# Kernel optimization log

Hardware: AMD Instinct MI355X
Metric: run time of the kernel (lower is better)

The kernel has to match this reference:

```python
import jax, jax.numpy as jnp
import numpy as np

N_NODES = 100000
N_EDGES = 1600000
IN_FEATS = 128
HIDDEN = 128
NUM_CLASSES = 2
EDGE_FEAT = 1


def setup_inputs() -> dict:
    key = jax.random.key(0)
    ks = jax.random.split(key, 24)
    s = 0.05
    inp = {
        "node_feats": jax.random.normal(ks[0], (N_NODES, IN_FEATS), jnp.float32),
        "edge_feats": jax.random.normal(ks[1], (N_EDGES, EDGE_FEAT), jnp.float32),
        "src": jax.random.randint(ks[2], (N_EDGES,), 0, N_NODES),
        "dst": jax.random.randint(ks[3], (N_EDGES,), 0, N_NODES),
        # SAGEConv layer 0: in -> hidden
        "ws0": jax.random.normal(ks[4], (IN_FEATS, HIDDEN), jnp.float32) * s,
        "wn0": jax.random.normal(ks[5], (IN_FEATS, HIDDEN), jnp.float32) * s,
        "b0": jnp.zeros((HIDDEN,), jnp.float32),
        # SAGEConv layer 1: hidden -> hidden
        "ws1": jax.random.normal(ks[6], (HIDDEN, HIDDEN), jnp.float32) * s,
        "wn1": jax.random.normal(ks[7], (HIDDEN, HIDDEN), jnp.float32) * s,
        "b1": jnp.zeros((HIDDEN,), jnp.float32),
        # SAGEConv layer 2: hidden -> hidden
        "ws2": jax.random.normal(ks[8], (HIDDEN, HIDDEN), jnp.float32) * s,
        "wn2": jax.random.normal(ks[9], (HIDDEN, HIDDEN), jnp.float32) * s,
        "b2": jnp.zeros((HIDDEN,), jnp.float32),
        # edge MLP
        "mw1": jax.random.normal(ks[10], (2 * HIDDEN + EDGE_FEAT, HIDDEN), jnp.float32) * s,
        "mb1": jnp.zeros((HIDDEN,), jnp.float32),
        "mw2": jax.random.normal(ks[11], (HIDDEN, NUM_CLASSES), jnp.float32) * s,
        "mb2": jnp.zeros((NUM_CLASSES,), jnp.float32),
    }
    return inp


def _sage_mean(h, src, dst, inv_deg, w_self, w_neigh, b, n_nodes):
    # mean over incoming edges of source features, per destination node
    agg = jax.ops.segment_sum(h[src], dst, num_segments=n_nodes)
    mean_neigh = agg * inv_deg
    return h @ w_self + mean_neigh @ w_neigh + b


def reference(node_feats, edge_feats, src, dst,
              ws0, wn0, b0, ws1, wn1, b1, ws2, wn2, b2,
              mw1, mb1, mw2, mb2):
    n_nodes = node_feats.shape[0]
    deg = jax.ops.segment_sum(jnp.ones_like(dst, dtype=node_feats.dtype), dst,
                              num_segments=n_nodes)
    inv_deg = (1.0 / jnp.maximum(deg, 1.0))[:, None]

    h = node_feats
    for (ws, wn, b) in ((ws0, wn0, b0), (ws1, wn1, b1), (ws2, wn2, b2)):
        h = _sage_mean(h, src, dst, inv_deg, ws, wn, b, n_nodes)
        h = jax.nn.leaky_relu(h, negative_slope=0.01)
        # dropout is identity in eval mode

    # edge gather + concat + MLP
    edge_repr = jnp.concatenate([h[src], h[dst], edge_feats], axis=1)
    hidden = jax.nn.relu(edge_repr @ mw1 + mb1)
    logits = hidden @ mw2 + mb2
    return logits
```

## Files before the change

kernel.cpp:

```cpp
#include <hip/hip_runtime.h>
#include <hip/hip_bf16.h>

#define N_NODES 100000
#define N_EDGES 1600000
#define F 128
#define KW 272
#define KS 144
#define KD 128
#define EROUNDS 8
#define NBUCK 512
#define BCAP 5120
#define NB 98
#define CHUNK 8192
#define NSBLK ((N_EDGES + CHUNK - 1) / CHUNK)

typedef short bf16x8 __attribute__((ext_vector_type(8)));
typedef float f32x16 __attribute__((ext_vector_type(16)));
typedef _Float16 half8 __attribute__((ext_vector_type(8)));
typedef _Float16 half4 __attribute__((ext_vector_type(4)));

__device__ __forceinline__ short f2bf(float x) {
    unsigned u = __builtin_bit_cast(unsigned, x);
    u += 0x7FFF + ((u >> 16) & 1);
    return (short)(u >> 16);
}
__device__ __forceinline__ float bflo(unsigned u) {
    return __builtin_bit_cast(float, u << 16);
}
__device__ __forceinline__ float bfhi(unsigned u) {
    return __builtin_bit_cast(float, u & 0xFFFF0000u);
}
__device__ __forceinline__ void acc8(float* a, uint4 u) {
    a[0] += bflo(u.x); a[1] += bfhi(u.x);
    a[2] += bflo(u.y); a[3] += bfhi(u.y);
    a[4] += bflo(u.z); a[5] += bfhi(u.z);
    a[6] += bflo(u.w); a[7] += bfhi(u.w);
}

__global__ __launch_bounds__(256) void bucket_scatter(
    const int* __restrict__ src, const int* __restrict__ dst,
    int* __restrict__ bcur, unsigned* __restrict__ bstore) {
    __shared__ int hist[NBUCK];
    __shared__ unsigned pk[CHUNK];
    int t = threadIdx.x;
    int e0 = blockIdx.x * CHUNK;
    int n = N_EDGES - e0; if (n > CHUNK) n = CHUNK;
    for (int i = t; i < NBUCK; i += 256) hist[i] = 0;
    __syncthreads();
    for (int i = t; i < n; i += 256) {
        int d = dst[e0 + i];
        int s = src[e0 + i];
        pk[i] = ((unsigned)(d & 255) << 17) | (unsigned)s;
        atomicAdd(&hist[d >> 8], 1);
    }
    __syncthreads();
    for (int i = t; i < NBUCK; i += 256) {
        int c = hist[i];
        hist[i] = (c > 0) ? atomicAdd(&bcur[i], c) : 0;
    }
    __syncthreads();
    for (int i = t; i < n; i += 256) {
        int bk = dst[e0 + i] >> 8;
        int p = atomicAdd(&hist[bk], 1);
        if (p < BCAP) bstore[(size_t)bk * BCAP + p] = pk[i];
    }
}

__global__ __launch_bounds__(256) void bucket_deg(const unsigned* __restrict__ bstore,
                                                  const int* __restrict__ bcur,
                                                  int* __restrict__ deg) {
    __shared__ int cnt[256];
    int b = blockIdx.x, t = threadIdx.x;
    cnt[t] = 0;
    __syncthreads();
    int n = bcur[b]; if (n > BCAP) n = BCAP;
    const unsigned* p = bstore + (size_t)b * BCAP;
    for (int i = t; i < n; i += 256) atomicAdd(&cnt[p[i] >> 17], 1);
    __syncthreads();
    int node = b * 256 + t;
    if (node < N_NODES) deg[node] = cnt[t];
}

__global__ __launch_bounds__(1024) void scan1_kernel(const int* __restrict__ deg,
                                                     int* __restrict__ incl,
                                                     int* __restrict__ bsum) {
    __shared__ int wsum[16];
    int t = threadIdx.x, lane = t & 63, wid = t >> 6;
    int i = blockIdx.x * 1024 + t;
    int v = (i < N_NODES) ? deg[i] : 0;
    int sc = v;
#pragma unroll
    for (int off = 1; off < 64; off <<= 1) {
        int u = __shfl_up(sc, off, 64);
        if (lane >= off) sc += u;
    }
    if (lane == 63) wsum[wid] = sc;
    __syncthreads();
    if (wid == 0) {
        int wv = (lane < 16) ? wsum[lane] : 0;
        int wi = wv;
#pragma unroll
        for (int off = 1; off < 16; off <<= 1) {
            int u = __shfl_up(wi, off, 64);
            if (lane >= off) wi += u;
        }
        if (lane < 16) wsum[lane] = wi - wv;
    }
    __syncthreads();
    int full = sc + wsum[wid];
    if (i < N_NODES) incl[i] = full;
    if (t == 1023) bsum[blockIdx.x] = full;
}

__global__ void scan2_kernel(const int* __restrict__ bsum, int* __restrict__ boff,
                             int* __restrict__ row_ptr) {
    __shared__ int w0;
    int t = threadIdx.x, lane = t & 63, wid = t >> 6;
    int v = (t < NB) ? bsum[t] : 0;
    int sc = v;
#pragma unroll
    for (int off = 1; off < 64; off <<= 1) {
        int u = __shfl_up(sc, off, 64);
        if (lane >= off) sc += u;
    }
    if (wid == 0 && lane == 63) w0 = sc;
    __syncthreads();
    if (wid == 1) sc += w0;
    if (t < NB) boff[t] = sc - v;
    if (t == NB - 1) row_ptr[N_NODES] = sc;
}

__global__ __launch_bounds__(1024) void scan3_kernel(const int* __restrict__ incl,
                                                     const int* __restrict__ deg,
                                                     const int* __restrict__ boff,
                                                     int* __restrict__ row_ptr,
                                                     float* __restrict__ invd) {
    int i = blockIdx.x * 1024 + threadIdx.x;
    if (i >= N_NODES) return;
    int d = deg[i];
    row_ptr[i] = incl[i] - d + boff[blockIdx.x];
    invd[i] = 1.0f / (float)(d > 1 ? d : 1);
}

__global__ __launch_bounds__(256) void bucket_fill(const unsigned* __restrict__ bstore,
                                                   const int* __restrict__ bcur,
                                                   const int* __restrict__ row_ptr,
                                                   int* __restrict__ csr_src) {
    __shared__ int cur[256];
    int b = blockIdx.x, t = threadIdx.x;
    int node = b * 256 + t;
    cur[t] = (node < N_NODES) ? row_ptr[node] : 0;
    __syncthreads();
    int n = bcur[b]; if (n > BCAP) n = BCAP;
    const unsigned* p = bstore + (size_t)b * BCAP;
    for (int i = t; i < n; i += 256) {
        unsigned e = p[i];
        int slot = atomicAdd(&cur[e >> 17], 1);
        csr_src[slot] = (int)(e & 0x1FFFF);
    }
}


__global__ void convert_bf16_kernel(const float* __restrict__ in, ushort* __restrict__ out) {
    int idx = (blockIdx.x * 256 + threadIdx.x) * 8;
    float4 a = *(const float4*)&in[idx];
    float4 b = *(const float4*)&in[idx + 4];
    ushort o[8];
    o[0] = (ushort)f2bf(a.x); o[1] = (ushort)f2bf(a.y);
    o[2] = (ushort)f2bf(a.z); o[3] = (ushort)f2bf(a.w);
    o[4] = (ushort)f2bf(b.x); o[5] = (ushort)f2bf(b.y);
    o[6] = (ushort)f2bf(b.z); o[7] = (ushort)f2bf(b.w);
    *(uint4*)&out[idx] = *(uint4*)o;
}


__global__ void prep_sage_w(const float* __restrict__ wsx, const float* __restrict__ wnx,
                            const float* __restrict__ b, ushort* __restrict__ aw) {
    int idx = blockIdx.x * 256 + threadIdx.x;
    if (idx >= 128 * KW) return;
    int h = idx / KW;
    int k = idx - h * KW;
    float v = 0.f;
    if (k < 128) v = wsx[(size_t)k * 128 + h];
    else if (k < 256) v = wnx[(size_t)(k - 128) * 128 + h];
    else if (k == 256) v = b[h];
    aw[idx] = (ushort)f2bf(v);
}

__global__ void prep_zs_w(const float* __restrict__ mw1, const float* __restrict__ mb1,
                          ushort* __restrict__ aw) {
    int idx = blockIdx.x * 256 + threadIdx.x;
    if (idx >= 128 * KS) return;
    int h = idx / KS;
    int k = idx - h * KS;
    float v = 0.f;
    if (k < 128) v = mw1[(size_t)k * 128 + h];
    else if (k == 128) v = mb1[h];
    aw[idx] = (ushort)f2bf(v);
}

__global__ void prep_zd_w(const float* __restrict__ mw1, ushort* __restrict__ aw) {
    int idx = blockIdx.x * 256 + threadIdx.x;
    if (idx >= 128 * KD) return;
    int h = idx / KD;
    int k = idx - h * KD;
    aw[idx] = (ushort)f2bf(mw1[(size_t)(128 + k) * 128 + h]);
}

__global__ __launch_bounds__(256) void agg_sage_fused(
    const ushort* __restrict__ hb, const int* __restrict__ csr_src,
    const int* __restrict__ row_ptr, const float* __restrict__ inv_deg,
    const ushort* __restrict__ aw, ushort* __restrict__ hout) {
    __shared__ ushort sM[32 * 136];
    int t = threadIdx.x;
    int lane = t & 63, w = t >> 6;
    int l31 = lane & 31, hf = lane >> 5;
    int slot = t >> 4;
    int fl = t & 15;

    int n0 = blockIdx.x * 32;
#pragma unroll
    for (int j = 0; j < 2; ++j) {
        int nb = j * 16 + slot;
        int node = n0 + nb;
        int s = row_ptr[node], e = row_ptr[node + 1];
        float acc[8] = {0.f, 0.f, 0.f, 0.f, 0.f, 0.f, 0.f, 0.f};
        int i = s;
        for (; i + 4 <= e; i += 4) {
            int m0 = csr_src[i], m1 = csr_src[i + 1], m2 = csr_src[i + 2], m3 = csr_src[i + 3];
            uint4 u0 = *(const uint4*)(hb + (size_t)m0 * F + fl * 8);
            uint4 u1 = *(const uint4*)(hb + (size_t)m1 * F + fl * 8);
            uint4 u2 = *(const uint4*)(hb + (size_t)m2 * F + fl * 8);
            uint4 u3 = *(const uint4*)(hb + (size_t)m3 * F + fl * 8);
            acc8(acc, u0); acc8(acc, u1); acc8(acc, u2); acc8(acc, u3);
        }
        for (; i < e; ++i) {
            int m = csr_src[i];
            uint4 u = *(const uint4*)(hb + (size_t)m * F + fl * 8);
            acc8(acc, u);
        }
        float iv = inv_deg[node];
        ushort o[8];
#pragma unroll
        for (int k = 0; k < 8; ++k) o[k] = (ushort)f2bf(acc[k] * iv);
        *(uint4*)&sM[nb * 136 + fl * 8] = *(uint4*)o;
    }

    bf16x8 afrag[17];
    const ushort* ap = aw + (size_t)(w * 32 + l31) * KW + hf * 8;
#pragma unroll
    for (int f = 0; f < 17; ++f) afrag[f] = *(const bf16x8*)(ap + f * 16);
    __syncthreads();

    int n = n0 + l31;
    const ushort* bs = hb + (size_t)n * F + hf * 8;
    f32x16 acc1, acc2;
#pragma unroll
    for (int r = 0; r < 16; ++r) { acc1[r] = 0.f; acc2[r] = 0.f; }
#pragma unroll
    for (int f = 0; f < 8; ++f) {
        bf16x8 b = *(const bf16x8*)(bs + f * 16);
        acc1 = __builtin_amdgcn_mfma_f32_32x32x16_bf16(afrag[f], b, acc1, 0, 0, 0);
    }
#pragma unroll
    for (int f = 0; f < 8; ++f) {
        bf16x8 b = *(const bf16x8*)&sM[l31 * 136 + hf * 8 + f * 16];
        acc2 = __builtin_amdgcn_mfma_f32_32x32x16_bf16(afrag[8 + f], b, acc2, 0, 0, 0);
    }
    bf16x8 bx;
#pragma unroll
    for (int j = 0; j < 8; ++j) bx[j] = 0;
    if (hf == 0) bx[0] = (short)0x3F80;
    acc2 = __builtin_amdgcn_mfma_f32_32x32x16_bf16(afrag[16], bx, acc2, 0, 0, 0);

#pragma unroll
    for (int g = 0; g < 4; ++g) {
        ushort o4[4];
#pragma unroll
        for (int j = 0; j < 4; ++j) {
            float v = acc1[g * 4 + j] + acc2[g * 4 + j];
            v = v > 0.f ? v : 0.01f * v;
            o4[j] = (ushort)f2bf(v);
        }
        *(uint2*)(hout + (size_t)n * F + w * 32 + g * 8 + hf * 4) = *(uint2*)o4;
    }
}

#define STILE 8
__global__ __launch_bounds__(256) void mlp_z_mfma(
    const ushort* __restrict__ hb, const ushort* __restrict__ aws,
    const ushort* __restrict__ awd, _Float16* __restrict__ zs,
    _Float16* __restrict__ zd) {
    int t = threadIdx.x;
    int lane = t & 63, w = t >> 6;
    int l31 = lane & 31, hf = lane >> 5;

    bf16x8 afs[9], afd[8];
    const ushort* aps = aws + (size_t)(w * 32 + l31) * KS + hf * 8;
    const ushort* apd = awd + (size_t)(w * 32 + l31) * KD + hf * 8;
#pragma unroll
    for (int f = 0; f < 9; ++f) afs[f] = *(const bf16x8*)(aps + f * 16);
#pragma unroll
    for (int f = 0; f < 8; ++f) afd[f] = *(const bf16x8*)(apd + f * 16);

    int tile0 = blockIdx.x * STILE;
    for (int tt = 0; tt < STILE; ++tt) {
        int tile = tile0 + tt;
        if (tile >= N_NODES / 32) break;
        int n = tile * 32 + l31;
        const ushort* bp = hb + (size_t)n * F + hf * 8;

        f32x16 accS, accD;
#pragma unroll
        for (int r = 0; r < 16; ++r) { accS[r] = 0.f; accD[r] = 0.f; }
#pragma unroll
        for (int f = 0; f < 8; ++f) {
            bf16x8 b = *(const bf16x8*)(bp + f * 16);
            accS = __builtin_amdgcn_mfma_f32_32x32x16_bf16(afs[f], b, accS, 0, 0, 0);
            accD = __builtin_amdgcn_mfma_f32_32x32x16_bf16(afd[f], b, accD, 0, 0, 0);
        }
        bf16x8 bx;
#pragma unroll
        for (int j = 0; j < 8; ++j) bx[j] = 0;
        if (hf == 0) bx[0] = (short)0x3F80;
        accS = __builtin_amdgcn_mfma_f32_32x32x16_bf16(afs[8], bx, accS, 0, 0, 0);

#pragma unroll
        for (int g = 0; g < 4; ++g) {
            half4 os, od;
#pragma unroll
            for (int j = 0; j < 4; ++j) {
                os[j] = (_Float16)accS[g * 4 + j];
                od[j] = (_Float16)accD[g * 4 + j];
            }
            int col = w * 32 + g * 8 + hf * 4;
            *(half4*)(zs + (size_t)n * F + col) = os;
            *(half4*)(zd + (size_t)n * F + col) = od;
        }
    }
}

__global__ __launch_bounds__(256) void edge_final(
    const _Float16* __restrict__ zs, const _Float16* __restrict__ zd,
    const float* __restrict__ ef,
    const int* __restrict__ src, const int* __restrict__ dst,
    const float* __restrict__ mw1, const float* __restrict__ mw2,
    const float* __restrict__ mb2, float* __restrict__ out) {
    int t = threadIdx.x;
    int g = t >> 4;
    int fl = t & 15;

    float wf[8], w2a[8], w2b[8];
#pragma unroll
    for (int j = 0; j < 8; ++j) {
        int feat = fl * 8 + j;
        wf[j]  = mw1[(size_t)256 * 128 + feat];
        float2 v = *(const float2*)&mw2[feat * 2];
        w2a[j] = v.x; w2b[j] = v.y;
    }
    float b20 = mb2[0], b21 = mb2[1];

    int e0 = blockIdx.x * (16 * EROUNDS);
    int isv[EROUNDS], idv[EROUNDS];
    float efv[EROUNDS];
#pragma unroll
    for (int r = 0; r < EROUNDS; ++r) {
        int e = e0 + r * 16 + g;
        isv[r] = src[e];
        idv[r] = dst[e];
        efv[r] = ef[e];
    }
#pragma unroll
    for (int r = 0; r < EROUNDS; ++r) {
        int e = e0 + r * 16 + g;
        half8 a = *(const half8*)(zs + (size_t)isv[r] * F + fl * 8);
        half8 b = *(const half8*)(zd + (size_t)idv[r] * F + fl * 8);
        float p0 = 0.f, p1 = 0.f;
#pragma unroll
        for (int j = 0; j < 8; ++j) {
            float v = (float)a[j] + (float)b[j] + efv[r] * wf[j];
            float hh = fmaxf(v, 0.f);
            p0 += hh * w2a[j];
            p1 += hh * w2b[j];
        }
#pragma unroll
        for (int m = 1; m < 16; m <<= 1) {
            p0 += __shfl_xor(p0, m, 64);
            p1 += __shfl_xor(p1, m, 64);
        }
        if (fl == 0) *(float2*)&out[(size_t)e * 2] = make_float2(p0 + b20, p1 + b21);
    }
}


extern "C" void kernel_launch(void* const* d_in, const int* in_sizes, int n_in,
                              void* d_out, int out_size, void* d_ws, size_t ws_size,
                              hipStream_t stream) {
    const float* node_feats = (const float*)d_in[0];
    const float* edge_feats = (const float*)d_in[1];
    const int*   src = (const int*)d_in[2];
    const int*   dst = (const int*)d_in[3];
    const float* ws0 = (const float*)d_in[4];
    const float* wn0 = (const float*)d_in[5];
    const float* b0  = (const float*)d_in[6];
    const float* ws1 = (const float*)d_in[7];
    const float* wn1 = (const float*)d_in[8];
    const float* b1  = (const float*)d_in[9];
    const float* ws2 = (const float*)d_in[10];
    const float* wn2 = (const float*)d_in[11];
    const float* b2  = (const float*)d_in[12];
    const float* mw1 = (const float*)d_in[13];
    const float* mb1 = (const float*)d_in[14];
    const float* mw2 = (const float*)d_in[15];
    const float* mb2 = (const float*)d_in[16];
    float* out = (float*)d_out;

    char* ws = (char*)d_ws;
    size_t off = 0;
    auto alloc = [&](size_t bytes) {
        size_t o = off;
        off += (bytes + 511) & ~(size_t)511;
        return o;
    };
    ushort* nfb = (ushort*)(ws + alloc((size_t)N_NODES * F * 2));
    ushort* hb0 = (ushort*)(ws + alloc((size_t)N_NODES * F * 2));
    ushort* hb1 = (ushort*)(ws + alloc((size_t)N_NODES * F * 2));
    ushort* zsb = (ushort*)(ws + alloc((size_t)N_NODES * F * 2));
    int*   deg  = (int*)  (ws + alloc((size_t)N_NODES * 4));
    float* invd = (float*)(ws + alloc((size_t)N_NODES * 4));
    int*   rowp = (int*)  (ws + alloc(((size_t)N_NODES + 1) * 4));
    int*   incl = (int*)  (ws + alloc((size_t)N_NODES * 4));
    int*   bsum = (int*)  (ws + alloc((size_t)NB * 4));
    int*   boff = (int*)  (ws + alloc((size_t)NB * 4));
    int*   csrc = (int*)  (ws + alloc((size_t)N_EDGES * 4));
    int*   bcur = (int*)  (ws + alloc((size_t)NBUCK * 4));
    unsigned* bstore = (unsigned*)(ws + alloc((size_t)NBUCK * BCAP * 4));
    ushort* aw0 = (ushort*)(ws + alloc((size_t)128 * KW * 2));
    ushort* aw1 = (ushort*)(ws + alloc((size_t)128 * KW * 2));
    ushort* aw2 = (ushort*)(ws + alloc((size_t)128 * KW * 2));
    ushort* awS = (ushort*)(ws + alloc((size_t)128 * KS * 2));
    ushort* awD = (ushort*)(ws + alloc((size_t)128 * KD * 2));
    _Float16* zs = (_Float16*)zsb;
    _Float16* zd = (_Float16*)nfb;

    hipMemsetAsync(bcur, 0, (size_t)NBUCK * 4, stream);
    bucket_scatter<<<NSBLK, 256, 0, stream>>>(src, dst, bcur, bstore);
    bucket_deg<<<NBUCK, 256, 0, stream>>>(bstore, bcur, deg);
    scan1_kernel<<<NB, 1024, 0, stream>>>(deg, incl, bsum);
    scan2_kernel<<<1, 128, 0, stream>>>(bsum, boff, rowp);
    scan3_kernel<<<NB, 1024, 0, stream>>>(incl, deg, boff, rowp, invd);
    bucket_fill<<<NBUCK, 256, 0, stream>>>(bstore, bcur, rowp, csrc);

    prep_sage_w<<<(128 * KW + 255) / 256, 256, 0, stream>>>(ws0, wn0, b0, aw0);
    prep_sage_w<<<(128 * KW + 255) / 256, 256, 0, stream>>>(ws1, wn1, b1, aw1);
    prep_sage_w<<<(128 * KW + 255) / 256, 256, 0, stream>>>(ws2, wn2, b2, aw2);
    prep_zs_w<<<(128 * KS + 255) / 256, 256, 0, stream>>>(mw1, mb1, awS);
    prep_zd_w<<<(128 * KD + 255) / 256, 256, 0, stream>>>(mw1, awD);
    convert_bf16_kernel<<<(N_NODES * F / 8 + 255) / 256, 256, 0, stream>>>(node_feats, nfb);

    const ushort* hin = nfb;
    ushort* houts[3] = {hb0, hb1, hb0};
    const ushort* aws_[3] = {aw0, aw1, aw2};
    for (int l = 0; l < 3; ++l) {
        agg_sage_fused<<<N_NODES / 32, 256, 0, stream>>>(hin, csrc, rowp, invd, aws_[l], houts[l]);
        hin = houts[l];
    }

    mlp_z_mfma<<<(N_NODES / 32 + STILE - 1) / STILE, 256, 0, stream>>>(hb0, awS, awD, zs, zd);
    edge_final<<<N_EDGES / (16 * EROUNDS), 256, 0, stream>>>(
        zs, zd, edge_feats, src, dst, mw1, mw2, mb2, out);
}
```

Baseline: 584.8 us.

## Fuse prep kernels, fuse edge-MLP projection into last SAGE layer, fp16 edge math

Merges the five weight-prep kernels and the bf16 input conversion into one launch. Fuses the per-node MLP projection (zs/zd) into the third SAGE layer by staging its output tile in shared memory, so the separate mlp_z kernel and the third layer's h write and re-read are gone. Unrolls the neighbour gather by 8 for more loads in flight, and moves the edge-final math to packed fp16 with fdot2. The fp16 arithmetic reduces precision, and the fused layer carries extra registers that may lower occupancy.

```diff
diff --git a/kernel.cpp b/kernel.cpp
--- a/kernel.cpp
+++ b/kernel.cpp
@@ -18,6 +18,7 @@
 typedef float f32x16 __attribute__((ext_vector_type(16)));
 typedef _Float16 half8 __attribute__((ext_vector_type(8)));
 typedef _Float16 half4 __attribute__((ext_vector_type(4)));
+typedef _Float16 half2v __attribute__((ext_vector_type(2)));
 
 __device__ __forceinline__ short f2bf(float x) {
     unsigned u = __builtin_bit_cast(unsigned, x);
@@ -160,57 +161,62 @@
     }
 }
 
-
-__global__ void convert_bf16_kernel(const float* __restrict__ in, ushort* __restrict__ out) {
-    int idx = (blockIdx.x * 256 + threadIdx.x) * 8;
-    float4 a = *(const float4*)&in[idx];
-    float4 b = *(const float4*)&in[idx + 4];
-    ushort o[8];
-    o[0] = (ushort)f2bf(a.x); o[1] = (ushort)f2bf(a.y);
-    o[2] = (ushort)f2bf(a.z); o[3] = (ushort)f2bf(a.w);
-    o[4] = (ushort)f2bf(b.x); o[5] = (ushort)f2bf(b.y);
-    o[6] = (ushort)f2bf(b.z); o[7] = (ushort)f2bf(b.w);
-    *(uint4*)&out[idx] = *(uint4*)o;
-}
-
-
-__global__ void prep_sage_w(const float* __restrict__ wsx, const float* __restrict__ wnx,
-                            const float* __restrict__ b, ushort* __restrict__ aw) {
-    int idx = blockIdx.x * 256 + threadIdx.x;
-    if (idx >= 128 * KW) return;
-    int h = idx / KW;
-    int k = idx - h * KW;
-    float v = 0.f;
-    if (k < 128) v = wsx[(size_t)k * 128 + h];
-    else if (k < 256) v = wnx[(size_t)(k - 128) * 128 + h];
-    else if (k == 256) v = b[h];
-    aw[idx] = (ushort)f2bf(v);
-}
-
-__global__ void prep_zs_w(const float* __restrict__ mw1, const float* __restrict__ mb1,
-                          ushort* __restrict__ aw) {
-    int idx = blockIdx.x * 256 + threadIdx.x;
-    if (idx >= 128 * KS) return;
-    int h = idx / KS;
-    int k = idx - h * KS;
-    float v = 0.f;
-    if (k < 128) v = mw1[(size_t)k * 128 + h];
-    else if (k == 128) v = mb1[h];
-    aw[idx] = (ushort)f2bf(v);
-}
-
-__global__ void prep_zd_w(const float* __restrict__ mw1, ushort* __restrict__ aw) {
-    int idx = blockIdx.x * 256 + threadIdx.x;
-    if (idx >= 128 * KD) return;
-    int h = idx / KD;
-    int k = idx - h * KD;
-    aw[idx] = (ushort)f2bf(mw1[(size_t)(128 + k) * 128 + h]);
-}
-
+__global__ __launch_bounds__(256) void prep_all(
+    const float* __restrict__ ws0, const float* __restrict__ wn0, const float* __restrict__ b0,
+    const float* __restrict__ ws1, const float* __restrict__ wn1, const float* __restrict__ b1,
+    const float* __restrict__ ws2, const float* __restrict__ wn2, const float* __restrict__ b2,
+    const float* __restrict__ mw1, const float* __restrict__ mb1,
+    ushort* __restrict__ aw0, ushort* __restrict__ aw1, ushort* __restrict__ aw2,
+    ushort* __restrict__ awS, ushort* __restrict__ awD,
+    const float* __restrict__ nf, ushort* __restrict__ nfb) {
+    int b = blockIdx.x, t = threadIdx.x;
+    if (b < 408) {
+        const float* wsx; const float* wnx; const float* bb; ushort* aw;
+        int rb;
+        if (b < 136)      { wsx = ws0; wnx = wn0; bb = b0; aw = aw0; rb = b; }
+        else if (b < 272) { wsx = ws1; wnx = wn1; bb = b1; aw = aw1; rb = b - 136; }
+        else              { wsx = ws2; wnx = wn2; bb = b2; aw = aw2; rb = b - 272; }
+        int idx = rb * 256 + t;
+        int h = idx / KW;
+        int k = idx - h * KW;
+        float v = 0.f;
+        if (k < 128) v = wsx[(size_t)k * 128 + h];
+        else if (k < 256) v = wnx[(size_t)(k - 128) * 128 + h];
+        else if (k == 256) v = bb[h];
+        aw[idx] = (ushort)f2bf(v);
+    } else if (b < 480) {
+        int idx = (b - 408) * 256 + t;
+        int h = idx / KS;
+        int k = idx - h * KS;
+        float v = 0.f;
+        if (k < 128) v = mw1[(size_t)k * 128 + h];
+        else if (k == 128) v = mb1[h];
+        awS[idx] = (ushort)f2bf(v);
+    } else if (b < 544) {
+        int idx = (b - 480) * 256 + t;
+        int h = idx >> 7;
+        int k = idx & 127;
+        awD[idx] = (ushort)f2bf(mw1[(size_t)(128 + k) * 128 + h]);
+    } else {
+        int idx = ((b - 544) * 256 + t) * 8;
+        float4 a = *(const float4*)&nf[idx];
+        float4 c = *(const float4*)&nf[idx + 4];
+        ushort o[8];
+        o[0] = (ushort)f2bf(a.x); o[1] = (ushort)f2bf(a.y);
+        o[2] = (ushort)f2bf(a.z); o[3] = (ushort)f2bf(a.w);
+        o[4] = (ushort)f2bf(c.x); o[5] = (ushort)f2bf(c.y);
+        o[6] = (ushort)f2bf(c.z); o[7] = (ushort)f2bf(c.w);
+        *(uint4*)&nfb[idx] = *(uint4*)o;
+    }
+}
+
+template <bool WITH_Z>
 __global__ __launch_bounds__(256) void agg_sage_fused(
     const ushort* __restrict__ hb, const int* __restrict__ csr_src,
     const int* __restrict__ row_ptr, const float* __restrict__ inv_deg,
-    const ushort* __restrict__ aw, ushort* __restrict__ hout) {
+    const ushort* __restrict__ aw, ushort* __restrict__ hout,
+    const ushort* __restrict__ aws, const ushort* __restrict__ awd,
+    _Float16* __restrict__ zs, _Float16* __restrict__ zd) {
     __shared__ ushort sM[32 * 136];
     int t = threadIdx.x;
     int lane = t & 63, w = t >> 6;
@@ -226,17 +232,27 @@
         int s = row_ptr[node], e = row_ptr[node + 1];
         float acc[8] = {0.f, 0.f, 0.f, 0.f, 0.f, 0.f, 0.f, 0.f};
         int i = s;
+        for (; i + 8 <= e; i += 8) {
+            uint4 u0 = *(const uint4*)(hb + (size_t)csr_src[i] * F + fl * 8);
+            uint4 u1 = *(const uint4*)(hb + (size_t)csr_src[i + 1] * F + fl * 8);
+            uint4 u2 = *(const uint4*)(hb + (size_t)csr_src[i + 2] * F + fl * 8);
+            uint4 u3 = *(const uint4*)(hb + (size_t)csr_src[i + 3] * F + fl * 8);
+            uint4 u4 = *(const uint4*)(hb + (size_t)csr_src[i + 4] * F + fl * 8);
+            uint4 u5 = *(const uint4*)(hb + (size_t)csr_src[i + 5] * F + fl * 8);
+            uint4 u6 = *(const uint4*)(hb + (size_t)csr_src[i + 6] * F + fl * 8);
+            uint4 u7 = *(const uint4*)(hb + (size_t)csr_src[i + 7] * F + fl * 8);
+            acc8(acc, u0); acc8(acc, u1); acc8(acc, u2); acc8(acc, u3);
+            acc8(acc, u4); acc8(acc, u5); acc8(acc, u6); acc8(acc, u7);
+        }
         for (; i + 4 <= e; i += 4) {
-            int m0 = csr_src[i], m1 = csr_src[i + 1], m2 = csr_src[i + 2], m3 = csr_src[i + 3];
-            uint4 u0 = *(const uint4*)(hb + (size_t)m0 * F + fl * 8);
-            uint4 u1 = *(const uint4*)(hb + (size_t)m1 * F + fl * 8);
-            uint4 u2 = *(const uint4*)(hb + (size_t)m2 * F + fl * 8);
-            uint4 u3 = *(const uint4*)(hb + (size_t)m3 * F + fl * 8);
+            uint4 u0 = *(const uint4*)(hb + (size_t)csr_src[i] * F + fl * 8);
+            uint4 u1 = *(const uint4*)(hb + (size_t)csr_src[i + 1] * F + fl * 8);
+            uint4 u2 = *(const uint4*)(hb + (size_t)csr_src[i + 2] * F + fl * 8);
+            uint4 u3 = *(const uint4*)(hb + (size_t)csr_src[i + 3] * F + fl * 8);
             acc8(acc, u0); acc8(acc, u1); acc8(acc, u2); acc8(acc, u3);
         }
         for (; i < e; ++i) {
-            int m = csr_src[i];
-            uint4 u = *(const uint4*)(hb + (size_t)m * F + fl * 8);
+            uint4 u = *(const uint4*)(hb + (size_t)csr_src[i] * F + fl * 8);
             acc8(acc, u);
         }
         float iv = inv_deg[node];
@@ -273,56 +289,54 @@
     if (hf == 0) bx[0] = (short)0x3F80;
     acc2 = __builtin_amdgcn_mfma_f32_32x32x16_bf16(afrag[16], bx, acc2, 0, 0, 0);
 
-#pragma unroll
-    for (int g = 0; g < 4; ++g) {
-        ushort o4[4];
-#pragma unroll
-        for (int j = 0; j < 4; ++j) {
-            float v = acc1[g * 4 + j] + acc2[g * 4 + j];
-            v = v > 0.f ? v : 0.01f * v;
-            o4[j] = (ushort)f2bf(v);
-        }
-        *(uint2*)(hout + (size_t)n * F + w * 32 + g * 8 + hf * 4) = *(uint2*)o4;
-    }
-}
-
-#define STILE 8
-__global__ __launch_bounds__(256) void mlp_z_mfma(
-    const ushort* __restrict__ hb, const ushort* __restrict__ aws,
-    const ushort* __restrict__ awd, _Float16* __restrict__ zs,
-    _Float16* __restrict__ zd) {
-    int t = threadIdx.x;
-    int lane = t & 63, w = t >> 6;
-    int l31 = lane & 31, hf = lane >> 5;
-
-    bf16x8 afs[9], afd[8];
-    const ushort* aps = aws + (size_t)(w * 32 + l31) * KS + hf * 8;
-    const ushort* apd = awd + (size_t)(w * 32 + l31) * KD + hf * 8;
-#pragma unroll
-    for (int f = 0; f < 9; ++f) afs[f] = *(const bf16x8*)(aps + f * 16);
-#pragma unroll
-    for (int f = 0; f < 8; ++f) afd[f] = *(const bf16x8*)(apd + f * 16);
-
-    int tile0 = blockIdx.x * STILE;
-    for (int tt = 0; tt < STILE; ++tt) {
-        int tile = tile0 + tt;
-        if (tile >= N_NODES / 32) break;
-        int n = tile * 32 + l31;
-        const ushort* bp = hb + (size_t)n * F + hf * 8;
+    if (!WITH_Z) {
+#pragma unroll
+        for (int g = 0; g < 4; ++g) {
+            ushort o4[4];
+#pragma unroll
+            for (int j = 0; j < 4; ++j) {
+                float v = acc1[g * 4 + j] + acc2[g * 4 + j];
+                v = v > 0.f ? v : 0.01f * v;
+                o4[j] = (ushort)f2bf(v);
+            }
+            *(uint2*)(hout + (size_t)n * F + w * 32 + g * 8 + hf * 4) = *(uint2*)o4;
+        }
+    } else {
+        uint2 hv[4];
+#pragma unroll
+        for (int g = 0; g < 4; ++g) {
+            ushort o4[4];
+#pragma unroll
+            for (int j = 0; j < 4; ++j) {
+                float v = acc1[g * 4 + j] + acc2[g * 4 + j];
+                v = v > 0.f ? v : 0.01f * v;
+                o4[j] = (ushort)f2bf(v);
+            }
+            hv[g] = *(uint2*)o4;
+        }
+        __syncthreads();
+#pragma unroll
+        for (int g = 0; g < 4; ++g)
+            *(uint2*)&sM[l31 * 136 + w * 32 + g * 8 + hf * 4] = hv[g];
+
+        bf16x8 afs[9], afd[8];
+        const ushort* aps = aws + (size_t)(w * 32 + l31) * KS + hf * 8;
+        const ushort* apd = awd + (size_t)(w * 32 + l31) * KD + hf * 8;
+#pragma unroll
+        for (int f = 0; f < 9; ++f) afs[f] = *(const bf16x8*)(aps + f * 16);
+#pragma unroll
+        for (int f = 0; f < 8; ++f) afd[f] = *(const bf16x8*)(apd + f * 16);
+        __syncthreads();
 
         f32x16 accS, accD;
 #pragma unroll
         for (int r = 0; r < 16; ++r) { accS[r] = 0.f; accD[r] = 0.f; }
 #pragma unroll
         for (int f = 0; f < 8; ++f) {
-            bf16x8 b = *(const bf16x8*)(bp + f * 16);
+            bf16x8 b = *(const bf16x8*)&sM[l31 * 136 + hf * 8 + f * 16];
             accS = __builtin_amdgcn_mfma_f32_32x32x16_bf16(afs[f], b, accS, 0, 0, 0);
             accD = __builtin_amdgcn_mfma_f32_32x32x16_bf16(afd[f], b, accD, 0, 0, 0);
         }
-        bf16x8 bx;
-#pragma unroll
-        for (int j = 0; j < 8; ++j) bx[j] = 0;
-        if (hf == 0) bx[0] = (short)0x3F80;
         accS = __builtin_amdgcn_mfma_f32_32x32x16_bf16(afs[8], bx, accS, 0, 0, 0);
 
 #pragma unroll
@@ -350,13 +364,20 @@
     int g = t >> 4;
     int fl = t & 15;
 
-    float wf[8], w2a[8], w2b[8];
+    half8 wf8;
+    half2v w2a2[4], w2b2[4];
 #pragma unroll
     for (int j = 0; j < 8; ++j) {
         int feat = fl * 8 + j;
-        wf[j]  = mw1[(size_t)256 * 128 + feat];
-        float2 v = *(const float2*)&mw2[feat * 2];
-        w2a[j] = v.x; w2b[j] = v.y;
+        wf8[j] = (_Float16)mw1[(size_t)256 * 128 + feat];
+    }
+#pragma unroll
+    for (int j = 0; j < 4; ++j) {
+        int feat = fl * 8 + 2 * j;
+        w2a2[j][0] = (_Float16)mw2[feat * 2];
+        w2a2[j][1] = (_Float16)mw2[(feat + 1) * 2];
+        w2b2[j][0] = (_Float16)mw2[feat * 2 + 1];
+        w2b2[j][1] = (_Float16)mw2[(feat + 1) * 2 + 1];
     }
     float b20 = mb2[0], b21 = mb2[1];
 
@@ -375,14 +396,26 @@
         int e = e0 + r * 16 + g;
         half8 a = *(const half8*)(zs + (size_t)isv[r] * F + fl * 8);
         half8 b = *(const half8*)(zd + (size_t)idv[r] * F + fl * 8);
+        _Float16 eh = (_Float16)efv[r];
+        half8 e8 = {eh, eh, eh, eh, eh, eh, eh, eh};
+        half8 v = a + b + wf8 * e8;
+        half8 zero = {0, 0, 0, 0, 0, 0, 0, 0};
+        v = __builtin_elementwise_max(v, zero);
         float p0 = 0.f, p1 = 0.f;
-#pragma unroll
-        for (int j = 0; j < 8; ++j) {
-            float v = (float)a[j] + (float)b[j] + efv[r] * wf[j];
-            float hh = fmaxf(v, 0.f);
-            p0 += hh * w2a[j];
-            p1 += hh * w2b[j];
-        }
+#if __has_builtin(__builtin_amdgcn_fdot2)
+#pragma unroll
+        for (int j = 0; j < 4; ++j) {
+            half2v hv = {v[2 * j], v[2 * j + 1]};
+            p0 = __builtin_amdgcn_fdot2(hv, w2a2[j], p0, false);
+            p1 = __builtin_amdgcn_fdot2(hv, w2b2[j], p1, false);
+        }
+#else
+#pragma unroll
+        for (int j = 0; j < 4; ++j) {
+            p0 += (float)v[2 * j] * (float)w2a2[j][0] + (float)v[2 * j + 1] * (float)w2a2[j][1];
+            p1 += (float)v[2 * j] * (float)w2b2[j][0] + (float)v[2 * j + 1] * (float)w2b2[j][1];
+        }
+#endif
 #pragma unroll
         for (int m = 1; m < 16; m <<= 1) {
             p0 += __shfl_xor(p0, m, 64);
@@ -451,22 +484,17 @@
     scan3_kernel<<<NB, 1024, 0, stream>>>(incl, deg, boff, rowp, invd);
     bucket_fill<<<NBUCK, 256, 0, stream>>>(bstore, bcur, rowp, csrc);
 
-    prep_sage_w<<<(128 * KW + 255) / 256, 256, 0, stream>>>(ws0, wn0, b0, aw0);
-    prep_sage_w<<<(128 * KW + 255) / 256, 256, 0, stream>>>(ws1, wn1, b1, aw1);
-    prep_sage_w<<<(128 * KW + 255) / 256, 256, 0, stream>>>(ws2, wn2, b2, aw2);
-    prep_zs_w<<<(128 * KS + 255) / 256, 256, 0, stream>>>(mw1, mb1, awS);
-    prep_zd_w<<<(128 * KD + 255) / 256, 256, 0, stream>>>(mw1, awD);
-    convert_bf16_kernel<<<(N_NODES * F / 8 + 255) / 256, 256, 0, stream>>>(node_feats, nfb);
-
-    const ushort* hin = nfb;
-    ushort* houts[3] = {hb0, hb1, hb0};
-    const ushort* aws_[3] = {aw0, aw1, aw2};
-    for (int l = 0; l < 3; ++l) {
-        agg_sage_fused<<<N_NODES / 32, 256, 0, stream>>>(hin, csrc, rowp, invd, aws_[l], houts[l]);
-        hin = houts[l];
-    }
-
-    mlp_z_mfma<<<(N_NODES / 32 + STILE - 1) / STILE, 256, 0, stream>>>(hb0, awS, awD, zs, zd);
+    prep_all<<<544 + N_NODES * F / 8 / 256, 256, 0, stream>>>(
+        ws0, wn0, b0, ws1, wn1, b1, ws2, wn2, b2, mw1, mb1,
+        aw0, aw1, aw2, awS, awD, node_feats, nfb);
+
+    agg_sage_fused<false><<<N_NODES / 32, 256, 0, stream>>>(
+        nfb, csrc, rowp, invd, aw0, hb0, nullptr, nullptr, nullptr, nullptr);
+    agg_sage_fused<false><<<N_NODES / 32, 256, 0, stream>>>(
+        hb0, csrc, rowp, invd, aw1, hb1, nullptr, nullptr, nullptr, nullptr);
+    agg_sage_fused<true><<<N_NODES / 32, 256, 0, stream>>>(
+        hb1, csrc, rowp, invd, aw2, hb0, awS, awD, zs, zd);
+
     edge_final<<<N_EDGES / (16 * EROUNDS), 256, 0, stream>>>(
         zs, zd, edge_feats, src, dst, mw1, mw2, mb2, out);
 }
```

Measured after the change: 546.8 us. 1.07x faster.
